# Optimization experiments

Hardware: AMD Instinct MI355X
Metric: run time of the kernel (lower is better)

Reference implementation:

```python
import jax, jax.numpy as jnp
import numpy as np

B, T, D, H = 4, 2048, 1024, 16
HD = D // H  # 64


def setup_inputs() -> dict:
    key = jax.random.key(0)
    k1, k2, k3 = jax.random.split(key, 3)
    x = jax.random.normal(k1, (B, T, D), dtype=jnp.float32)
    # xavier-uniform-ish scaling for stability
    W_qkv = jax.random.normal(k2, (3 * D, D), dtype=jnp.float32) * (1.0 / np.sqrt(D))
    W_proj = jax.random.normal(k3, (D, D), dtype=jnp.float32) * (1.0 / np.sqrt(D))
    b_proj = jnp.zeros((D,), dtype=jnp.float32)
    return {"x": x, "W_qkv": W_qkv, "W_proj": W_proj, "b_proj": b_proj}


def reference(x, W_qkv, W_proj, b_proj):
    Bx, Tx, C = x.shape
    qkv = x @ W_qkv.T                      # [B,T,3C]
    q, k, v = jnp.split(qkv, 3, axis=-1)
    # [B,T,C] -> [B,H,T,hd]
    def heads(t):
        return t.reshape(Bx, Tx, H, HD).transpose(0, 2, 1, 3)
    q, k, v = heads(q), heads(k), heads(v)
    scale = 1.0 / np.sqrt(HD)
    scores = jnp.einsum('bhqd,bhkd->bhqk', q, k) * scale  # [B,H,T,T]
    causal = jnp.tril(jnp.ones((Tx, Tx), dtype=bool))
    scores = jnp.where(causal, scores, jnp.finfo(scores.dtype).min)
    attn = jax.nn.softmax(scores, axis=-1)
    out = jnp.einsum('bhqk,bhkd->bhqd', attn, v)          # [B,H,T,hd]
    out = out.transpose(0, 2, 1, 3).reshape(Bx, Tx, C)    # [B,T,C]
    return out @ W_proj.T + b_proj
```

## Files before the change

kernel.cpp:

```cpp
#include <hip/hip_runtime.h>
#include <hip/hip_bf16.h>

#define B_  4
#define T_  2048
#define D_  1024
#define H_  16
#define HD_ 64
#define THREE_D (3 * D_)
#define TWO_D   (2 * D_)

typedef short s16x8 __attribute__((ext_vector_type(8)));
typedef short s16x4 __attribute__((ext_vector_type(4)));
typedef float f32x4 __attribute__((ext_vector_type(4)));
typedef unsigned int u32x2 __attribute__((ext_vector_type(2)));
typedef unsigned short u16;
typedef unsigned short u16x4 __attribute__((ext_vector_type(4)));

static __device__ __forceinline__ s16x8 load8(const u16* p) {
    return *reinterpret_cast<const s16x8*>(p);
}
static __device__ __forceinline__ u16 f2bf(float f) {
    __hip_bfloat16 h = __float2bfloat16(f);
    return *reinterpret_cast<u16*>(&h);
}
static __device__ __forceinline__ unsigned cvtpk(float lo, float hi) {
    float2 f; f.x = lo; f.y = hi;
    __hip_bfloat162 h = __float22bfloat162_rn(f);
    return *reinterpret_cast<unsigned*>(&h);
}
static __device__ __forceinline__ void mfma16(f32x4& d, u16x4 a, u16x4 b) {
#if __has_builtin(__builtin_amdgcn_mfma_f32_16x16x16bf16_1k)
    d = __builtin_amdgcn_mfma_f32_16x16x16bf16_1k(
        __builtin_bit_cast(s16x4, a), __builtin_bit_cast(s16x4, b), d, 0, 0, 0);
#else
    asm volatile("s_nop 1\n\t"
                 "v_mfma_f32_16x16x16_bf16 %0, %1, %2, %0\n\t"
                 "s_nop 7\n\t"
                 "s_nop 3"
                 : "+v"(d) : "v"(a), "v"(b));
#endif
}

static __device__ __forceinline__ void gload_lds16(const u16* g, u16* l) {
#if __has_builtin(__builtin_amdgcn_global_load_lds)
    __builtin_amdgcn_global_load_lds(
        (__attribute__((address_space(1))) void*)g,
        (__attribute__((address_space(3))) void*)l, 16, 0, 0);
#else
    *reinterpret_cast<s16x8*>(l) = load8(g);
#endif
}

__global__ __launch_bounds__(256) void cvt_f32_bf16(
    const float* __restrict__ in, u16* __restrict__ out, int n)
{
    const int i = (blockIdx.x * 256 + threadIdx.x) * 4;
    if (i < n) {
        const float4 f = *reinterpret_cast<const float4*>(in + i);
        u16x4 r;
        r.x = f2bf(f.x); r.y = f2bf(f.y); r.z = f2bf(f.z); r.w = f2bf(f.w);
        *reinterpret_cast<u16x4*>(out + i) = r;
    }
}

template<int MODE>
__global__ __launch_bounds__(256) void gemm_bt128(
    const u16* __restrict__ A,
    const u16* __restrict__ Bm,
    void* __restrict__ Cv,
    const float* __restrict__ bias,
    int M, int N, int K, int lda, int ldb, int ldc,
    float qsc, u16* __restrict__ vt)
{
    const int ntiles = N >> 7;
    const int mt = blockIdx.x / ntiles;
    const int nt = blockIdx.x % ntiles;
    const int m0 = mt * 128, n0 = nt * 128;
    const int tid  = threadIdx.x;
    const int lane = tid & 63;
    const int l15  = lane & 15;
    const int quad = lane >> 4;
    const int wave = tid >> 6;
    const int wm = (wave >> 1) * 64;
    const int wn = (wave & 1) * 64;

    __shared__ u16 A_sh[2][128 * 32];
    __shared__ u16 B_sh[2][128 * 32];

    f32x4 acc[4][4] = {};

    const int c0 = tid, c1 = tid + 256;
    const int ar0 = c0 >> 2, as0 = (c0 & 3) * 8;
    const int ar1 = c1 >> 2, as1 = (c1 & 3) * 8;
    const u16* Ag0 = A  + (size_t)(m0 + ar0) * lda + as0;
    const u16* Ag1 = A  + (size_t)(m0 + ar1) * lda + as1;
    const u16* Bg0 = Bm + (size_t)(n0 + ar0) * ldb + as0;
    const u16* Bg1 = Bm + (size_t)(n0 + ar1) * ldb + as1;

    for (int k0 = 0; k0 < K; k0 += 64) {
        __syncthreads();
        #pragma unroll
        for (int p = 0; p < 2; ++p) {
            gload_lds16(Ag0 + k0 + p * 32, &A_sh[p][c0 * 8]);
            gload_lds16(Ag1 + k0 + p * 32, &A_sh[p][c1 * 8]);
            gload_lds16(Bg0 + k0 + p * 32, &B_sh[p][c0 * 8]);
            gload_lds16(Bg1 + k0 + p * 32, &B_sh[p][c1 * 8]);
        }
        __syncthreads();

        #pragma unroll
        for (int p = 0; p < 2; ++p) {
            s16x8 a[4], b[4];
            #pragma unroll
            for (int i = 0; i < 4; ++i) {
                a[i] = *reinterpret_cast<const s16x8*>(&A_sh[p][(wm + i * 16 + l15) * 32 + quad * 8]);
                b[i] = *reinterpret_cast<const s16x8*>(&B_sh[p][(wn + i * 16 + l15) * 32 + quad * 8]);
            }
            #pragma unroll
            for (int mi = 0; mi < 4; ++mi)
                #pragma unroll
                for (int ni = 0; ni < 4; ++ni)
                    acc[mi][ni] = __builtin_amdgcn_mfma_f32_16x16x32_bf16(
                        a[mi], b[ni], acc[mi][ni], 0, 0, 0);
        }
    }

    #pragma unroll
    for (int ni = 0; ni < 4; ++ni) {
        const int col = n0 + wn + ni * 16 + l15;
        if (MODE == 0) {
            const float bv = bias ? bias[col] : 0.0f;
            #pragma unroll
            for (int mi = 0; mi < 4; ++mi) {
                const int row = m0 + wm + mi * 16 + quad * 4;
                #pragma unroll
                for (int r = 0; r < 4; ++r)
                    ((float*)Cv)[(size_t)(row + r) * ldc + col] = acc[mi][ni][r] + bv;
            }
        } else {
            if (col < TWO_D) {
                const float sc = (col < D_) ? qsc : 1.0f;
                #pragma unroll
                for (int mi = 0; mi < 4; ++mi) {
                    const int row = m0 + wm + mi * 16 + quad * 4;
                    #pragma unroll
                    for (int r = 0; r < 4; ++r)
                        ((u16*)Cv)[(size_t)(row + r) * ldc + col] = f2bf(acc[mi][ni][r] * sc);
                }
            } else {
                const int vc = col - TWO_D;
                #pragma unroll
                for (int mi = 0; mi < 4; ++mi) {
                    const int row = m0 + wm + mi * 16 + quad * 4;
                    const int bb = row >> 11, t = row & (T_ - 1);
                    u16x4 pk;
                    #pragma unroll
                    for (int r = 0; r < 4; ++r) pk[r] = f2bf(acc[mi][ni][r]);
                    *reinterpret_cast<u16x4*>(
                        vt + ((size_t)(bb * H_ * HD_) + vc) * T_ + t) = pk;
                }
            }
        }
    }
}

__global__ __launch_bounds__(256) void flash_attn9(
    const u16* __restrict__ qk, const u16* __restrict__ vt,
    u16* __restrict__ out)
{
    const int cls = blockIdx.x >> 6;
    const int bh  = blockIdx.x & 63;
    const int qmap[16] = {15,14,13,12, 8,9,10,11, 7,6,5,4, 0,1,2,3};
    const int qt = qmap[cls];
    const int h = bh & 15, b = bh >> 4;
    const int q0 = qt * 128;

    __shared__ u16 K_lds[64 * 72];
    __shared__ u16 V_lds[64 * 72];

    const int tid = threadIdx.x;
    const int wave = tid >> 6, lane = tid & 63;
    const int l15 = lane & 15, quad = lane >> 4;

    const int w0 = q0 + wave * 32;

    s16x8 qf[2][2];
    #pragma unroll
    for (int mi = 0; mi < 2; ++mi) {
        const size_t rowQ = (size_t)(b * T_ + w0 + mi * 16 + l15) * TWO_D + h * HD_;
        qf[mi][0] = load8(qk + rowQ + quad * 8);
        qf[mi][1] = load8(qk + rowQ + 32 + quad * 8);
    }

    f32x4 o[2][4] = {};
    f32x4 osum[2] = {};

    u16x4 ones4;
    #pragma unroll
    for (int j = 0; j < 4; ++j) ones4[j] = 0x3F80;

    const int r0 = tid >> 3;
    const int s0 = (tid & 7) * 8;
    const u16* Kg0 = qk + (size_t)(b * T_ + r0)      * TWO_D + D_ + h * HD_ + s0;
    const u16* Kg1 = qk + (size_t)(b * T_ + r0 + 32) * TWO_D + D_ + h * HD_ + s0;
    const u16* Vg0 = vt + (size_t)(bh * HD_ + r0)      * T_ + s0;
    const u16* Vg1 = vt + (size_t)(bh * HD_ + r0 + 32) * T_ + s0;

    s16x8 pk0 = load8(Kg0);
    s16x8 pk1 = load8(Kg1);
    s16x8 pv0 = load8(Vg0);
    s16x8 pv1 = load8(Vg1);

    const int nkt = 2 * qt + 2;
    for (int kt = 0; kt < nkt; ++kt) {
        const int kbase = kt * 64;
        __syncthreads();
        *reinterpret_cast<s16x8*>(&K_lds[r0 * 72 + s0])        = pk0;
        *reinterpret_cast<s16x8*>(&K_lds[(r0 + 32) * 72 + s0]) = pk1;
        *reinterpret_cast<s16x8*>(&V_lds[r0 * 72 + s0])        = pv0;
        *reinterpret_cast<s16x8*>(&V_lds[(r0 + 32) * 72 + s0]) = pv1;
        __syncthreads();

        if (kt + 1 < nkt) {
            const int nb = kbase + 64;
            pk0 = load8(Kg0 + (size_t)nb * TWO_D);
            pk1 = load8(Kg1 + (size_t)nb * TWO_D);
            pv0 = load8(Vg0 + nb);
            pv1 = load8(Vg1 + nb);
        }

        if (kbase <= w0 + 31) {
            f32x4 st[2][4];
            #pragma unroll
            for (int n = 0; n < 4; ++n) {
                const s16x8 kf0 = *reinterpret_cast<const s16x8*>(
                    &K_lds[(n * 16 + l15) * 72 + quad * 8]);
                const s16x8 kf1 = *reinterpret_cast<const s16x8*>(
                    &K_lds[(n * 16 + l15) * 72 + 32 + quad * 8]);
                #pragma unroll
                for (int mi = 0; mi < 2; ++mi) {
                    f32x4 t = {};
                    t = __builtin_amdgcn_mfma_f32_16x16x32_bf16(kf0, qf[mi][0], t, 0, 0, 0);
                    t = __builtin_amdgcn_mfma_f32_16x16x32_bf16(kf1, qf[mi][1], t, 0, 0, 0);
                    st[mi][n] = t;
                }
            }

            const bool diag = (kbase + 63 > w0);
            u16x4 pa[2][4];
            #pragma unroll
            for (int mi = 0; mi < 2; ++mi) {
                const int qr = w0 + mi * 16 + l15;
                #pragma unroll
                for (int n = 0; n < 4; ++n) {
                    const int kb = kbase + n * 16 + quad * 4;
                    float e0 = exp2f(st[mi][n][0]);
                    float e1 = exp2f(st[mi][n][1]);
                    float e2 = exp2f(st[mi][n][2]);
                    float e3 = exp2f(st[mi][n][3]);
                    if (diag) {
                        if (kb + 0 > qr) e0 = 0.0f;
                        if (kb + 1 > qr) e1 = 0.0f;
                        if (kb + 2 > qr) e2 = 0.0f;
                        if (kb + 3 > qr) e3 = 0.0f;
                    }
                    u32x2 w; w.x = cvtpk(e0, e1); w.y = cvtpk(e2, e3);
                    pa[mi][n] = __builtin_bit_cast(u16x4, w);
                }
            }

            #pragma unroll
            for (int n = 0; n < 4; ++n) {
                #pragma unroll
                for (int mi = 0; mi < 2; ++mi)
                    mfma16(osum[mi], pa[mi][n], ones4);
                #pragma unroll
                for (int n4 = 0; n4 < 4; ++n4) {
                    const u16x4 vb = *reinterpret_cast<const u16x4*>(
                        &V_lds[(n4 * 16 + l15) * 72 + n * 16 + quad * 4]);
                    #pragma unroll
                    for (int mi = 0; mi < 2; ++mi)
                        mfma16(o[mi][n4], pa[mi][n], vb);
                }
            }
        }
    }

    #pragma unroll
    for (int mi = 0; mi < 2; ++mi)
        #pragma unroll
        for (int r = 0; r < 4; ++r) {
            const float inv = 1.0f / osum[mi][r];
            const size_t rowO = (size_t)(b * T_ + w0 + mi * 16 + quad * 4 + r) * D_ + h * HD_;
            #pragma unroll
            for (int n4 = 0; n4 < 4; ++n4)
                out[rowO + n4 * 16 + l15] = f2bf(o[mi][n4][r] * inv);
        }
}

extern "C" void kernel_launch(void* const* d_in, const int* in_sizes, int n_in,
                              void* d_out, int out_size, void* d_ws, size_t ws_size,
                              hipStream_t stream)
{
    const float* x     = (const float*)d_in[0];
    const float* Wqkv  = (const float*)d_in[1];
    const float* Wproj = (const float*)d_in[2];
    const float* bproj = (const float*)d_in[3];
    float* out = (float*)d_out;

    const int M = B_ * T_;
    const float cs = 0.18033688011f;

    u16* xb    = (u16*)d_ws;
    u16* wqkvb = xb    + (size_t)M * D_;
    u16* wprob = wqkvb + (size_t)THREE_D * D_;
    u16* qk    = wprob + (size_t)D_ * D_;
    u16* vtb   = qk    + (size_t)M * TWO_D;
    u16* attn  = vtb   + (size_t)B_ * H_ * HD_ * T_;

    {
        int n;
        n = M * D_;
        cvt_f32_bf16<<<dim3((n / 4 + 255) / 256), 256, 0, stream>>>(x, xb, n);
        n = THREE_D * D_;
        cvt_f32_bf16<<<dim3((n / 4 + 255) / 256), 256, 0, stream>>>(Wqkv, wqkvb, n);
        n = D_ * D_;
        cvt_f32_bf16<<<dim3((n / 4 + 255) / 256), 256, 0, stream>>>(Wproj, wprob, n);
    }

    gemm_bt128<1><<<dim3((M / 128) * (THREE_D / 128)), 256, 0, stream>>>(
        xb, wqkvb, qk, nullptr, M, THREE_D, D_, D_, D_, TWO_D, cs, vtb);

    flash_attn9<<<dim3(B_ * H_ * (T_ / 128)), 256, 0, stream>>>(qk, vtb, attn);

    gemm_bt128<0><<<dim3((M / 128) * (D_ / 128)), 256, 0, stream>>>(
        attn, wprob, out, bproj, M, D_, D_, D_, D_, D_, 1.0f, nullptr);
}
```

Measured before the change: 266.1 us.

## Drop LDS staging in attention, load K/V fragments directly from global

The attention kernel no longer stages K and V tiles through shared memory with block barriers. Each wave now reads its MFMA fragments straight from global memory, relying on L1/L2 for reuse across the four waves. Each wave's loop count now follows its own causal extent instead of the block's, so waves skip tiles they never use. The bf16 packing of probabilities switches from round-to-nearest conversion to truncation via a byte permute, which is cheaper but slightly less accurate. The risks are more global traffic, small uncoalesced 8-byte V loads, and exposed load latency now that the software prefetch is gone.

```diff
diff --git a/kernel.cpp b/kernel.cpp
--- a/kernel.cpp
+++ b/kernel.cpp
@@ -23,10 +23,15 @@
     __hip_bfloat16 h = __float2bfloat16(f);
     return *reinterpret_cast<u16*>(&h);
 }
-static __device__ __forceinline__ unsigned cvtpk(float lo, float hi) {
-    float2 f; f.x = lo; f.y = hi;
-    __hip_bfloat162 h = __float22bfloat162_rn(f);
-    return *reinterpret_cast<unsigned*>(&h);
+static __device__ __forceinline__ unsigned pktrunc(float lo, float hi) {
+#if __has_builtin(__builtin_amdgcn_perm)
+    return __builtin_amdgcn_perm(__builtin_bit_cast(unsigned, hi),
+                                 __builtin_bit_cast(unsigned, lo),
+                                 0x07060302u);
+#else
+    return (__builtin_bit_cast(unsigned, hi) & 0xFFFF0000u) |
+           (__builtin_bit_cast(unsigned, lo) >> 16);
+#endif
 }
 static __device__ __forceinline__ void mfma16(f32x4& d, u16x4 a, u16x4 b) {
 #if __has_builtin(__builtin_amdgcn_mfma_f32_16x16x16bf16_1k)
@@ -164,7 +169,7 @@
     }
 }
 
-__global__ __launch_bounds__(256) void flash_attn9(
+__global__ __launch_bounds__(256) void flash_attn10(
     const u16* __restrict__ qk, const u16* __restrict__ vt,
     u16* __restrict__ out)
 {
@@ -175,13 +180,9 @@
     const int h = bh & 15, b = bh >> 4;
     const int q0 = qt * 128;
 
-    __shared__ u16 K_lds[64 * 72];
-    __shared__ u16 V_lds[64 * 72];
-
     const int tid = threadIdx.x;
     const int wave = tid >> 6, lane = tid & 63;
     const int l15 = lane & 15, quad = lane >> 4;
-
     const int w0 = q0 + wave * 32;
 
     s16x8 qf[2][2];
@@ -199,89 +200,64 @@
     #pragma unroll
     for (int j = 0; j < 4; ++j) ones4[j] = 0x3F80;
 
-    const int r0 = tid >> 3;
-    const int s0 = (tid & 7) * 8;
-    const u16* Kg0 = qk + (size_t)(b * T_ + r0)      * TWO_D + D_ + h * HD_ + s0;
-    const u16* Kg1 = qk + (size_t)(b * T_ + r0 + 32) * TWO_D + D_ + h * HD_ + s0;
-    const u16* Vg0 = vt + (size_t)(bh * HD_ + r0)      * T_ + s0;
-    const u16* Vg1 = vt + (size_t)(bh * HD_ + r0 + 32) * T_ + s0;
-
-    s16x8 pk0 = load8(Kg0);
-    s16x8 pk1 = load8(Kg1);
-    s16x8 pv0 = load8(Vg0);
-    s16x8 pv1 = load8(Vg1);
-
-    const int nkt = 2 * qt + 2;
+    const u16* Kb = qk + (size_t)(b * T_ + l15) * TWO_D + D_ + h * HD_ + quad * 8;
+    const u16* Vb = vt + (size_t)(bh * HD_ + l15) * T_ + quad * 4;
+
+    const int nkt = ((w0 + 31) >> 6) + 1;
     for (int kt = 0; kt < nkt; ++kt) {
         const int kbase = kt * 64;
-        __syncthreads();
-        *reinterpret_cast<s16x8*>(&K_lds[r0 * 72 + s0])        = pk0;
-        *reinterpret_cast<s16x8*>(&K_lds[(r0 + 32) * 72 + s0]) = pk1;
-        *reinterpret_cast<s16x8*>(&V_lds[r0 * 72 + s0])        = pv0;
-        *reinterpret_cast<s16x8*>(&V_lds[(r0 + 32) * 72 + s0]) = pv1;
-        __syncthreads();
-
-        if (kt + 1 < nkt) {
-            const int nb = kbase + 64;
-            pk0 = load8(Kg0 + (size_t)nb * TWO_D);
-            pk1 = load8(Kg1 + (size_t)nb * TWO_D);
-            pv0 = load8(Vg0 + nb);
-            pv1 = load8(Vg1 + nb);
-        }
-
-        if (kbase <= w0 + 31) {
-            f32x4 st[2][4];
+        const u16* Kt = Kb + (size_t)kbase * TWO_D;
+        const u16* Vt = Vb + kbase;
+
+        f32x4 st[2][4];
+        #pragma unroll
+        for (int n = 0; n < 4; ++n) {
+            const s16x8 kf0 = load8(Kt + (size_t)(n * 16) * TWO_D);
+            const s16x8 kf1 = load8(Kt + (size_t)(n * 16) * TWO_D + 32);
+            #pragma unroll
+            for (int mi = 0; mi < 2; ++mi) {
+                f32x4 t = {};
+                t = __builtin_amdgcn_mfma_f32_16x16x32_bf16(kf0, qf[mi][0], t, 0, 0, 0);
+                t = __builtin_amdgcn_mfma_f32_16x16x32_bf16(kf1, qf[mi][1], t, 0, 0, 0);
+                st[mi][n] = t;
+            }
+        }
+
+        const bool diag = (kbase + 63 > w0);
+        u16x4 pa[2][4];
+        #pragma unroll
+        for (int mi = 0; mi < 2; ++mi) {
+            const int qr = w0 + mi * 16 + l15;
             #pragma unroll
             for (int n = 0; n < 4; ++n) {
-                const s16x8 kf0 = *reinterpret_cast<const s16x8*>(
-                    &K_lds[(n * 16 + l15) * 72 + quad * 8]);
-                const s16x8 kf1 = *reinterpret_cast<const s16x8*>(
-                    &K_lds[(n * 16 + l15) * 72 + 32 + quad * 8]);
-                #pragma unroll
-                for (int mi = 0; mi < 2; ++mi) {
-                    f32x4 t = {};
-                    t = __builtin_amdgcn_mfma_f32_16x16x32_bf16(kf0, qf[mi][0], t, 0, 0, 0);
-                    t = __builtin_amdgcn_mfma_f32_16x16x32_bf16(kf1, qf[mi][1], t, 0, 0, 0);
-                    st[mi][n] = t;
+                const int kb = kbase + n * 16 + quad * 4;
+                float e0 = exp2f(st[mi][n][0]);
+                float e1 = exp2f(st[mi][n][1]);
+                float e2 = exp2f(st[mi][n][2]);
+                float e3 = exp2f(st[mi][n][3]);
+                if (diag) {
+                    if (kb + 0 > qr) e0 = 0.0f;
+                    if (kb + 1 > qr) e1 = 0.0f;
+                    if (kb + 2 > qr) e2 = 0.0f;
+                    if (kb + 3 > qr) e3 = 0.0f;
                 }
-            }
-
-            const bool diag = (kbase + 63 > w0);
-            u16x4 pa[2][4];
-            #pragma unroll
-            for (int mi = 0; mi < 2; ++mi) {
-                const int qr = w0 + mi * 16 + l15;
-                #pragma unroll
-                for (int n = 0; n < 4; ++n) {
-                    const int kb = kbase + n * 16 + quad * 4;
-                    float e0 = exp2f(st[mi][n][0]);
-                    float e1 = exp2f(st[mi][n][1]);
-                    float e2 = exp2f(st[mi][n][2]);
-                    float e3 = exp2f(st[mi][n][3]);
-                    if (diag) {
-                        if (kb + 0 > qr) e0 = 0.0f;
-                        if (kb + 1 > qr) e1 = 0.0f;
-                        if (kb + 2 > qr) e2 = 0.0f;
-                        if (kb + 3 > qr) e3 = 0.0f;
-                    }
-                    u32x2 w; w.x = cvtpk(e0, e1); w.y = cvtpk(e2, e3);
-                    pa[mi][n] = __builtin_bit_cast(u16x4, w);
-                }
-            }
-
-            #pragma unroll
-            for (int n = 0; n < 4; ++n) {
+                u32x2 w; w.x = pktrunc(e0, e1); w.y = pktrunc(e2, e3);
+                pa[mi][n] = __builtin_bit_cast(u16x4, w);
+            }
+        }
+
+        #pragma unroll
+        for (int n = 0; n < 4; ++n) {
+            #pragma unroll
+            for (int mi = 0; mi < 2; ++mi)
+                mfma16(osum[mi], pa[mi][n], ones4);
+            #pragma unroll
+            for (int n4 = 0; n4 < 4; ++n4) {
+                const u16x4 vb = *reinterpret_cast<const u16x4*>(
+                    Vt + (size_t)(n4 * 16) * T_ + n * 16);
                 #pragma unroll
                 for (int mi = 0; mi < 2; ++mi)
-                    mfma16(osum[mi], pa[mi][n], ones4);
-                #pragma unroll
-                for (int n4 = 0; n4 < 4; ++n4) {
-                    const u16x4 vb = *reinterpret_cast<const u16x4*>(
-                        &V_lds[(n4 * 16 + l15) * 72 + n * 16 + quad * 4]);
-                    #pragma unroll
-                    for (int mi = 0; mi < 2; ++mi)
-                        mfma16(o[mi][n4], pa[mi][n], vb);
-                }
+                    mfma16(o[mi][n4], pa[mi][n], vb);
             }
         }
     }
@@ -331,7 +307,7 @@
     gemm_bt128<1><<<dim3((M / 128) * (THREE_D / 128)), 256, 0, stream>>>(
         xb, wqkvb, qk, nullptr, M, THREE_D, D_, D_, D_, TWO_D, cs, vtb);
 
-    flash_attn9<<<dim3(B_ * H_ * (T_ / 128)), 256, 0, stream>>>(qk, vtb, attn);
+    flash_attn10<<<dim3(B_ * H_ * (T_ / 128)), 256, 0, stream>>>(qk, vtb, attn);
 
     gemm_bt128<0><<<dim3((M / 128) * (D_ / 128)), 256, 0, stream>>>(
         attn, wprob, out, bproj, M, D_, D_, D_, D_, D_, 1.0f, nullptr);
```

Result: slower. 385.5 us (+44.9%).
